# Performance work log

Hardware: AMD Instinct MI355X
Metric: run time of the kernel (lower is better)

## Reference

```python
import jax, jax.numpy as jnp
import numpy as np

N_NODES = 100000
N_EDGES = 3200000
N_GRAPHS = 2048
MOL_DIM = 78
HID = 32
OUT = 128
N_LAYERS = 5
BN_EPS = 1e-5


def setup_inputs() -> dict:
    key = jax.random.key(0)
    ks = jax.random.split(key, 16)
    x = jax.random.normal(ks[0], (N_NODES, MOL_DIM), dtype=jnp.float32)
    edge_index = jax.random.randint(ks[1], (2, N_EDGES), 0, N_NODES, dtype=jnp.int32)
    batch = jnp.sort(jax.random.randint(ks[2], (N_NODES,), 0, N_GRAPHS, dtype=jnp.int32))
    def lin(k, fan_in, shape):
        b = 1.0 / np.sqrt(fan_in)
        return jax.random.uniform(k, shape, jnp.float32, -b, b)
    # layer 0 MLP (78 -> 32 -> 32)
    w1_0 = lin(ks[3], MOL_DIM, (MOL_DIM, HID))
    b1_0 = lin(ks[4], MOL_DIM, (HID,))
    w2_0 = lin(ks[5], HID, (HID, HID))
    b2_0 = lin(ks[6], HID, (HID,))
    # layers 1..4 MLPs (32 -> 32 -> 32), stacked
    w1 = lin(ks[7], HID, (N_LAYERS - 1, HID, HID))
    b1 = lin(ks[8], HID, (N_LAYERS - 1, HID))
    w2 = lin(ks[9], HID, (N_LAYERS - 1, HID, HID))
    b2 = lin(ks[10], HID, (N_LAYERS - 1, HID))
    # BatchNorm affine params per layer
    gamma = jnp.ones((N_LAYERS, HID), jnp.float32)
    beta = jnp.zeros((N_LAYERS, HID), jnp.float32)
    # final fc (32 -> 128)
    fc_w = lin(ks[11], HID, (HID, OUT))
    fc_b = lin(ks[12], HID, (OUT,))
    return {"x": x, "edge_index": edge_index, "batch": batch,
            "w1_0": w1_0, "b1_0": b1_0, "w2_0": w2_0, "b2_0": b2_0,
            "w1": w1, "b1": b1, "w2": w2, "b2": b2,
            "gamma": gamma, "beta": beta, "fc_w": fc_w, "fc_b": fc_b}


def _gin_layer(x, src, dst, W1, B1, W2, B2, g, bt):
    # GIN aggregation: (1+eps)*x + sum_{j in N(i)} x_j, eps = 0
    agg = x + jax.ops.segment_sum(x[src], dst, num_segments=N_NODES)
    h = jnp.maximum(agg @ W1 + B1, 0.0)   # Linear + ReLU
    h = h @ W2 + B2                        # Linear
    h = jnp.maximum(h, 0.0)                # outer act before BN
    mean = jnp.mean(h, axis=0)
    var = jnp.mean(jnp.square(h - mean), axis=0)  # biased (training BN)
    return (h - mean) * jax.lax.rsqrt(var + BN_EPS) * g + bt


def reference(x, edge_index, batch, w1_0, b1_0, w2_0, b2_0,
              w1, b1, w2, b2, gamma, beta, fc_w, fc_b):
    src, dst = edge_index[0], edge_index[1]
    h = _gin_layer(x, src, dst, w1_0, b1_0, w2_0, b2_0, gamma[0], beta[0])
    for i in range(N_LAYERS - 1):
        h = _gin_layer(h, src, dst, w1[i], b1[i], w2[i], b2[i],
                       gamma[i + 1], beta[i + 1])
    pooled = jax.ops.segment_sum(h, batch, num_segments=N_GRAPHS)  # [G, HID]
    out = jnp.maximum(pooled @ fc_w + fc_b, 0.0)  # dropout is identity in eval
    return out
```

## Files before the change

kernel.cpp:

```cpp
#include <hip/hip_runtime.h>
#include <hip/hip_fp16.h>

#define N_NODES 100000
#define N_EDGES 3200000
#define N_GRAPHS 2048
#define MOL 78
#define HID 32
#define OUTD 128
#define BN_EPS 1e-5f

#define NBUCK ((N_NODES + 255) / 256)
#define BCAP2 9216
#define EPB 4096
#define P1_BLOCKS ((N_EDGES + EPB - 1) / EPB)

#define NPH 4
#define CPL_BLOCKS (N_NODES / (8 * NPH))

#define NCOPY 64

__device__ inline unsigned int pkh2(float a, float b) {
    __half2 h = __halves2half2(__float2half_rn(a), __float2half_rn(b));
    return *(unsigned int*)&h;
}
__device__ inline float hlo(unsigned int v) {
    __half2 h = *(__half2*)&v;
    return __low2float(h);
}
__device__ inline float hhi(unsigned int v) {
    __half2 h = *(__half2*)&v;
    return __high2float(h);
}


__global__ __launch_bounds__(256) void part1_kernel(const int* __restrict__ src,
                                                    const int* __restrict__ dst,
                                                    int* __restrict__ gcur,
                                                    int* __restrict__ staging) {
    __shared__ int hist[NBUCK];
    __shared__ int lofs[NBUCK];
    __shared__ int lcur[NBUCK];
    __shared__ int gb[NBUCK];
    __shared__ int pk[EPB];
    __shared__ unsigned short bkt[EPB];
    __shared__ int sc[256];
    const int t = threadIdx.x;
    const int base = blockIdx.x * EPB;
    const int nedge = min(EPB, N_EDGES - base);

    for (int i = t; i < NBUCK; i += 256) hist[i] = 0;
    __syncthreads();
    for (int i = t; i < nedge; i += 256) atomicAdd(&hist[dst[base + i] >> 8], 1);
    __syncthreads();

    int a0 = (2 * t < NBUCK) ? hist[2 * t] : 0;
    int a1 = (2 * t + 1 < NBUCK) ? hist[2 * t + 1] : 0;
    int tot = a0 + a1;
    sc[t] = tot;
    __syncthreads();
    for (int off = 1; off < 256; off <<= 1) {
        int add = (t >= off) ? sc[t - off] : 0;
        __syncthreads();
        sc[t] += add;
        __syncthreads();
    }
    int excl = sc[t] - tot;
    if (2 * t < NBUCK) { lofs[2 * t] = excl; lcur[2 * t] = excl; }
    if (2 * t + 1 < NBUCK) { lofs[2 * t + 1] = excl + a0; lcur[2 * t + 1] = excl + a0; }
    __syncthreads();

    for (int i = t; i < nedge; i += 256) {
        int d = dst[base + i];
        int s = src[base + i];
        int b = d >> 8;
        int p = atomicAdd(&lcur[b], 1);
        pk[p] = (s << 8) | (d & 255);
        bkt[p] = (unsigned short)b;
    }
    __syncthreads();

    for (int b = t; b < NBUCK; b += 256) {
        int c = lcur[b] - lofs[b];
        gb[b] = c ? atomicAdd(&gcur[b], c) : 0;
    }
    __syncthreads();

    for (int i = t; i < nedge; i += 256) {
        int b = bkt[i];
        staging[(size_t)b * BCAP2 + gb[b] + (i - lofs[b])] = pk[i];
    }
}

__global__ void csrbase_kernel(const int* __restrict__ gcur, int* __restrict__ bbase,
                               int* __restrict__ row_start) {
    int t = threadIdx.x;
    int a0 = (2 * t < NBUCK) ? gcur[2 * t] : 0;
    int a1 = (2 * t + 1 < NBUCK) ? gcur[2 * t + 1] : 0;
    int tot = a0 + a1;
    __shared__ int sc[256];
    sc[t] = tot;
    __syncthreads();
    for (int off = 1; off < 256; off <<= 1) {
        int add = (t >= off) ? sc[t - off] : 0;
        __syncthreads();
        sc[t] += add;
        __syncthreads();
    }
    int excl = sc[t] - tot;
    if (2 * t < NBUCK) bbase[2 * t] = excl;
    if (2 * t + 1 < NBUCK) bbase[2 * t + 1] = excl + a0;
    if (t == 0) row_start[N_NODES] = N_EDGES;
}

__global__ __launch_bounds__(256) void part2_kernel(const int* __restrict__ gcur,
                                                    const int* __restrict__ bbase,
                                                    const int* __restrict__ staging,
                                                    int* __restrict__ row_start,
                                                    int* __restrict__ csr,
                                                    float* __restrict__ degf) {
    int b = blockIdx.x, t = threadIdx.x;
    __shared__ int ldeg[256];
    __shared__ int lex[256];
    __shared__ int sc[256];
    ldeg[t] = 0;
    __syncthreads();
    int cnt = gcur[b];
    int base = bbase[b];
    const int* sp = staging + (size_t)b * BCAP2;
    for (int i = t; i < cnt; i += 256) atomicAdd(&ldeg[sp[i] & 255], 1);
    __syncthreads();
    int v = ldeg[t];
    sc[t] = v;
    __syncthreads();
    for (int off = 1; off < 256; off <<= 1) {
        int add = (t >= off) ? sc[t - off] : 0;
        __syncthreads();
        sc[t] += add;
        __syncthreads();
    }
    int excl = sc[t] - v;
    int node = b * 256 + t;
    if (node < N_NODES) {
        row_start[node] = base + excl;
        degf[node] = 1.0f + (float)v;
    }
    lex[t] = base + excl;
    __syncthreads();
    for (int i = t; i < cnt; i += 256) {
        int pk = sp[i];
        int p = atomicAdd(&lex[pk & 255], 1);
        csr[p] = pk >> 8;
    }
}


__global__ void gcnt_kernel(const int* __restrict__ batch, int* __restrict__ cnt) {
    int g = blockIdx.x * blockDim.x + threadIdx.x;
    if (g >= N_GRAPHS) return;
    auto lb = [&](int key) {
        int lo = 0, hi = N_NODES;
        while (lo < hi) {
            int mid = (lo + hi) >> 1;
            if (batch[mid] < key) lo = mid + 1; else hi = mid;
        }
        return lo;
    };
    cnt[g] = lb(g + 1) - lb(g);
}


__global__ __launch_bounds__(256) void proj78_kernel(const float* __restrict__ in,
                                                     const float* __restrict__ W1,
                                                     unsigned int* __restrict__ y) {
    __shared__ float w1s[MOL * HID];
    for (int i = threadIdx.x; i < MOL * HID; i += 256) w1s[i] = W1[i];
    __syncthreads();
    const int node = blockIdx.x * 256 + threadIdx.x;
    if (node >= N_NODES) return;
    const float* row = in + (size_t)node * MOL;
    float acc[HID];
#pragma unroll
    for (int j = 0; j < HID; j++) acc[j] = 0.f;
    const float4* w1v = (const float4*)w1s;
    for (int k = 0; k < MOL; k++) {
        float xv = row[k];
#pragma unroll
        for (int q = 0; q < 8; q++) {
            float4 wv = w1v[k * 8 + q];
            acc[4 * q + 0] = fmaf(xv, wv.x, acc[4 * q + 0]);
            acc[4 * q + 1] = fmaf(xv, wv.y, acc[4 * q + 1]);
            acc[4 * q + 2] = fmaf(xv, wv.z, acc[4 * q + 2]);
            acc[4 * q + 3] = fmaf(xv, wv.w, acc[4 * q + 3]);
        }
    }
    uint4* o = (uint4*)(y + (size_t)node * 16);
#pragma unroll
    for (int g = 0; g < 4; g++) {
        uint4 u;
        u.x = pkh2(acc[8 * g + 0], acc[8 * g + 1]);
        u.y = pkh2(acc[8 * g + 2], acc[8 * g + 3]);
        u.z = pkh2(acc[8 * g + 4], acc[8 * g + 5]);
        u.w = pkh2(acc[8 * g + 6], acc[8 * g + 7]);
        o[g] = u;
    }
}


__global__ __launch_bounds__(256) void agg_kernel(const unsigned int* __restrict__ y,
                                                  const int* __restrict__ rs,
                                                  const int* __restrict__ csr,
                                                  float* __restrict__ agg) {
    int gt = blockIdx.x * blockDim.x + threadIdx.x;
    int node = gt >> 5;
    if (node >= N_NODES) return;
    int hl = threadIdx.x & 31;
    int s = hl >> 2;
    int q = hl & 3;
    const uint4* rows = (const uint4*)y;
    float acc[8];
#pragma unroll
    for (int i = 0; i < 8; i++) acc[i] = 0.f;
    if (s == 0) {
        uint4 u = rows[(size_t)node * 4 + q];
        acc[0] = hlo(u.x); acc[1] = hhi(u.x);
        acc[2] = hlo(u.y); acc[3] = hhi(u.y);
        acc[4] = hlo(u.z); acc[5] = hhi(u.z);
        acc[6] = hlo(u.w); acc[7] = hhi(u.w);
    }
    int e0 = rs[node], e1 = rs[node + 1];
    int k = e0 + s;
    for (; k + 8 < e1; k += 16) {
        uint4 a = rows[(size_t)csr[k] * 4 + q];
        uint4 b = rows[(size_t)csr[k + 8] * 4 + q];
        acc[0] += hlo(a.x) + hlo(b.x);
        acc[1] += hhi(a.x) + hhi(b.x);
        acc[2] += hlo(a.y) + hlo(b.y);
        acc[3] += hhi(a.y) + hhi(b.y);
        acc[4] += hlo(a.z) + hlo(b.z);
        acc[5] += hhi(a.z) + hhi(b.z);
        acc[6] += hlo(a.w) + hlo(b.w);
        acc[7] += hhi(a.w) + hhi(b.w);
    }
    if (k < e1) {
        uint4 a = rows[(size_t)csr[k] * 4 + q];
        acc[0] += hlo(a.x); acc[1] += hhi(a.x);
        acc[2] += hlo(a.y); acc[3] += hhi(a.y);
        acc[4] += hlo(a.z); acc[5] += hhi(a.z);
        acc[6] += hlo(a.w); acc[7] += hhi(a.w);
    }
#pragma unroll
    for (int m = 4; m <= 16; m <<= 1) {
#pragma unroll
        for (int i = 0; i < 8; i++) acc[i] += __shfl_xor(acc[i], m, 32);
    }
    if (s == 0) {
        float4* o = (float4*)(agg + (size_t)node * HID + q * 8);
        o[0] = make_float4(acc[0], acc[1], acc[2], acc[3]);
        o[1] = make_float4(acc[4], acc[5], acc[6], acc[7]);
    }
}


__global__ __launch_bounds__(256) void mlp2cpl_kernel(const float* __restrict__ agg,
                                                      const float* __restrict__ B1,
                                                      const float* __restrict__ W2,
                                                      const float* __restrict__ B2,
                                                      __half* __restrict__ out,
                                                      float* __restrict__ sums) {
    __shared__ float ldsv[8][NPH][HID];
    __shared__ float ssum[64];
    const int t = threadIdx.x;
    const int hw = t >> 5;
    const int c = t & 31;
    if (t < 64) ssum[t] = 0.f;
    float w2col[32];
#pragma unroll
    for (int k = 0; k < 32; k++) w2col[k] = W2[k * 32 + c];
    const float b1c = B1[c], b2c = B2[c];
    const int n0 = (blockIdx.x * 8 + hw) * NPH;
#pragma unroll
    for (int u = 0; u < NPH; u++) {
        float v = fmaxf(agg[(size_t)(n0 + u) * 32 + c] + b1c, 0.f);
        ldsv[hw][u][c] = v;
    }
    __syncthreads();
    float sl = 0.f, sq = 0.f;
#pragma unroll
    for (int u = 0; u < NPH; u++) {
        float h = b2c;
        const float4* vv4 = (const float4*)&ldsv[hw][u][0];
#pragma unroll
        for (int q = 0; q < 8; q++) {
            float4 vv = vv4[q];
            h = fmaf(vv.x, w2col[4 * q + 0], h);
            h = fmaf(vv.y, w2col[4 * q + 1], h);
            h = fmaf(vv.z, w2col[4 * q + 2], h);
            h = fmaf(vv.w, w2col[4 * q + 3], h);
        }
        h = fmaxf(h, 0.f);
        out[(size_t)(n0 + u) * 32 + c] = __float2half_rn(h);
        sl += h;
        sq += h * h;
    }
    atomicAdd(&ssum[c], sl);
    atomicAdd(&ssum[32 + c], sq);
    __syncthreads();
    if (t < 64) atomicAdd(&sums[(blockIdx.x & (NCOPY - 1)) * 64 + t], ssum[t]);
}


template <bool LAST>
__global__ __launch_bounds__(256) void fusedmlp_kernel(
    const float* __restrict__ aggh, const float* __restrict__ degf,
    const float* __restrict__ scsh_prev, const float* __restrict__ B1,
    const float* __restrict__ W1, const float* __restrict__ W2, const float* __restrict__ B2,
    __half* __restrict__ out, float* __restrict__ sums, const int* __restrict__ batch,
    float* __restrict__ pooledraw) {
    __shared__ float ldsu[8][NPH][HID];
    __shared__ float ldsv[8][HID];
    __shared__ float ssum[64];
    const int t = threadIdx.x;
    const int hw = t >> 5;
    const int c = t & 31;
    if (t < 64) ssum[t] = 0.f;
    float w1col[32], w2col[32];
#pragma unroll
    for (int k = 0; k < 32; k++) {
        w1col[k] = W1[k * 32 + c];
        w2col[k] = W2[k * 32 + c];
    }
    const float scv = scsh_prev[c], shv = scsh_prev[HID + c];
    const float b1c = B1[c], b2c = B2[c];
    const int n0 = (blockIdx.x * 8 + hw) * NPH;
#pragma unroll
    for (int u = 0; u < NPH; u++) {
        int n = n0 + u;
        float cdeg = degf[n];
        ldsu[hw][u][c] = fmaf(aggh[(size_t)n * 32 + c], scv, cdeg * shv);
    }
    __syncthreads();
    float sl = 0.f, sq = 0.f;
#pragma unroll
    for (int u = 0; u < NPH; u++) {
        const int n = n0 + u;
        float tv = b1c;
        const float4* uu4 = (const float4*)&ldsu[hw][u][0];
#pragma unroll
        for (int q = 0; q < 8; q++) {
            float4 uu = uu4[q];
            tv = fmaf(uu.x, w1col[4 * q + 0], tv);
            tv = fmaf(uu.y, w1col[4 * q + 1], tv);
            tv = fmaf(uu.z, w1col[4 * q + 2], tv);
            tv = fmaf(uu.w, w1col[4 * q + 3], tv);
        }
        tv = fmaxf(tv, 0.f);
        ldsv[hw][c] = tv;
        float h = b2c;
        const float4* vv4 = (const float4*)&ldsv[hw][0];
#pragma unroll
        for (int q = 0; q < 8; q++) {
            float4 vv = vv4[q];
            h = fmaf(vv.x, w2col[4 * q + 0], h);
            h = fmaf(vv.y, w2col[4 * q + 1], h);
            h = fmaf(vv.z, w2col[4 * q + 2], h);
            h = fmaf(vv.w, w2col[4 * q + 3], h);
        }
        h = fmaxf(h, 0.f);
        if (LAST) {
            atomicAdd(&pooledraw[batch[n] * HID + c], h);
        } else {
            out[(size_t)n * 32 + c] = __float2half_rn(h);
        }
        sl += h;
        sq += h * h;
    }
    atomicAdd(&ssum[c], sl);
    atomicAdd(&ssum[32 + c], sq);
    __syncthreads();
    if (t < 64) atomicAdd(&sums[(blockIdx.x & (NCOPY - 1)) * 64 + t], ssum[t]);
}


__global__ void bnfin_kernel(const float* __restrict__ sums, const float* __restrict__ g,
                             const float* __restrict__ bt, float* __restrict__ scsh) {
    __shared__ float red[64];
    int t = threadIdx.x;
    if (t < 64) {
        float acc = 0.f;
#pragma unroll 8
        for (int k = 0; k < NCOPY; k++) acc += sums[k * 64 + t];
        red[t] = acc;
    }
    __syncthreads();
    if (t < HID) {
        float m = red[t] * (1.0f / N_NODES);
        float var = red[HID + t] * (1.0f / N_NODES) - m * m;
        var = fmaxf(var, 0.f);
        float sc = g[t] * rsqrtf(var + BN_EPS);
        scsh[t] = sc;
        scsh[HID + t] = bt[t] - m * sc;
    }
}


__global__ void fc_kernel(const float* __restrict__ praw, const int* __restrict__ cnt,
                          const float* __restrict__ scsh4, const float* __restrict__ fcw,
                          const float* __restrict__ fcb, float* __restrict__ out) {
    __shared__ float w[HID * OUTD];
    __shared__ float aff[2 * HID];
    for (int i = threadIdx.x; i < HID * OUTD; i += 256) w[i] = fcw[i];
    if (threadIdx.x < 2 * HID) aff[threadIdx.x] = scsh4[threadIdx.x];
    __syncthreads();
    int idx = blockIdx.x * 256 + threadIdx.x;
    if (idx >= N_GRAPHS * OUTD) return;
    int g = idx >> 7;
    int o = idx & 127;
    float cg = (float)cnt[g];
    float acc = fcb[o];
#pragma unroll
    for (int k = 0; k < HID; k++) {
        float paff = fmaf(praw[g * HID + k], aff[k], cg * aff[HID + k]);
        acc = fmaf(paff, w[k * OUTD + o], acc);
    }
    out[idx] = fmaxf(acc, 0.f);
}


extern "C" void kernel_launch(void* const* d_in, const int* in_sizes, int n_in,
                              void* d_out, int out_size, void* d_ws, size_t ws_size,
                              hipStream_t stream) {
    const float* x = (const float*)d_in[0];
    const int* ei = (const int*)d_in[1];
    const int* batch = (const int*)d_in[2];
    const float* w1_0 = (const float*)d_in[3];
    const float* b1_0 = (const float*)d_in[4];
    const float* w2_0 = (const float*)d_in[5];
    const float* b2_0 = (const float*)d_in[6];
    const float* w1 = (const float*)d_in[7];
    const float* b1 = (const float*)d_in[8];
    const float* w2 = (const float*)d_in[9];
    const float* b2 = (const float*)d_in[10];
    const float* gamma = (const float*)d_in[11];
    const float* beta = (const float*)d_in[12];
    const float* fc_w = (const float*)d_in[13];
    const float* fc_b = (const float*)d_in[14];
    float* out = (float*)d_out;

    const int* e_src = ei;
    const int* e_dst = ei + N_EDGES;

    char* ws = (char*)d_ws;
    size_t off = 0;
    auto alloc = [&](size_t n) {
        void* p = ws + off;
        off += (n + 255) & ~(size_t)255;
        return p;
    };
    int* row_start = (int*)alloc((size_t)(N_NODES + 1) * 4);
    int* csr = (int*)alloc((size_t)N_EDGES * 4);
    int* bbase = (int*)alloc((size_t)NBUCK * 4);
    int* staging = (int*)alloc((size_t)NBUCK * BCAP2 * 4);
    unsigned int* ybuf = (unsigned int*)alloc((size_t)N_NODES * 16 * 4);
    float* aggb = (float*)alloc((size_t)N_NODES * HID * 4);
    __half* hbuf = (__half*)alloc((size_t)N_NODES * HID * 2);
    float* degf = (float*)alloc((size_t)N_NODES * 4);
    float* scsh = (float*)alloc(5 * 2 * HID * 4);
    int* cnt = (int*)alloc((size_t)N_GRAPHS * 4);
    size_t zero_base = off;
    int* gcur = (int*)alloc((size_t)NBUCK * 4);
    float* bnsums = (float*)alloc((size_t)5 * NCOPY * 64 * 4);
    float* pooled = (float*)alloc((size_t)N_GRAPHS * HID * 4);
    size_t zero_len = off - zero_base;

    hipMemsetAsync(ws + zero_base, 0, zero_len, stream);

    part1_kernel<<<P1_BLOCKS, 256, 0, stream>>>(e_src, e_dst, gcur, staging);
    csrbase_kernel<<<1, 256, 0, stream>>>(gcur, bbase, row_start);
    part2_kernel<<<NBUCK, 256, 0, stream>>>(gcur, bbase, staging, row_start, csr, degf);
    gcnt_kernel<<<(N_GRAPHS + 255) / 256, 256, 0, stream>>>(batch, cnt);

    const int nodeBlocks = (N_NODES + 255) / 256;
    const int aggBlocks = (N_NODES * 32 + 255) / 256;

    proj78_kernel<<<nodeBlocks, 256, 0, stream>>>(x, w1_0, ybuf);
    agg_kernel<<<aggBlocks, 256, 0, stream>>>(ybuf, row_start, csr, aggb);
    mlp2cpl_kernel<<<CPL_BLOCKS, 256, 0, stream>>>(aggb, b1_0, w2_0, b2_0, hbuf, bnsums);
    bnfin_kernel<<<1, 64, 0, stream>>>(bnsums, gamma, beta, scsh);

    for (int l = 1; l < 5; l++) {
        int i = l - 1;
        agg_kernel<<<aggBlocks, 256, 0, stream>>>((const unsigned int*)hbuf, row_start, csr,
                                                  aggb);
        if (l < 4) {
            fusedmlp_kernel<false><<<CPL_BLOCKS, 256, 0, stream>>>(
                aggb, degf, scsh + (l - 1) * 2 * HID, b1 + (size_t)i * HID,
                w1 + (size_t)i * HID * HID, w2 + (size_t)i * HID * HID, b2 + (size_t)i * HID,
                hbuf, bnsums + (size_t)l * NCOPY * 64, nullptr, nullptr);
        } else {
            fusedmlp_kernel<true><<<CPL_BLOCKS, 256, 0, stream>>>(
                aggb, degf, scsh + (l - 1) * 2 * HID, b1 + (size_t)i * HID,
                w1 + (size_t)i * HID * HID, w2 + (size_t)i * HID * HID, b2 + (size_t)i * HID,
                nullptr, bnsums + (size_t)l * NCOPY * 64, batch, pooled);
        }
        bnfin_kernel<<<1, 64, 0, stream>>>(bnsums + (size_t)l * NCOPY * 64, gamma + l * HID,
                                           beta + l * HID, scsh + l * 2 * HID);
    }

    fc_kernel<<<(N_GRAPHS * OUTD + 255) / 256, 256, 0, stream>>>(
        pooled, cnt, scsh + 4 * 2 * HID, fc_w, fc_b, out);
}
```

Baseline: 424.4 us.

## Fuse neighbor aggregation into per-layer MLP kernel with ping-pong fp16 buffers

Merges the separate gather-sum aggregation kernel into the MLP/BatchNorm-statistics kernel. Each half-wave now gathers its 4 nodes' neighbors and writes the BN-adjusted or bias+ReLU row straight into shared memory. This removes the fp32 aggregation buffer round trip through global memory and one launch per layer, and alternates two fp16 feature buffers between layers. In exchange, each half-wave processes its nodes' gathers one after another, which may reduce memory-level parallelism. The removed block barrier before the shared-sum atomics also introduces a possible race on their initialisation.

```diff
diff --git a/kernel.cpp b/kernel.cpp
--- a/kernel.cpp
+++ b/kernel.cpp
@@ -206,167 +206,150 @@
 }
 
 
-__global__ __launch_bounds__(256) void agg_kernel(const unsigned int* __restrict__ y,
-                                                  const int* __restrict__ rs,
-                                                  const int* __restrict__ csr,
-                                                  float* __restrict__ agg) {
-    int gt = blockIdx.x * blockDim.x + threadIdx.x;
-    int node = gt >> 5;
-    if (node >= N_NODES) return;
-    int hl = threadIdx.x & 31;
-    int s = hl >> 2;
-    int q = hl & 3;
-    const uint4* rows = (const uint4*)y;
-    float acc[8];
-#pragma unroll
-    for (int i = 0; i < 8; i++) acc[i] = 0.f;
-    if (s == 0) {
-        uint4 u = rows[(size_t)node * 4 + q];
-        acc[0] = hlo(u.x); acc[1] = hhi(u.x);
-        acc[2] = hlo(u.y); acc[3] = hhi(u.y);
-        acc[4] = hlo(u.z); acc[5] = hhi(u.z);
-        acc[6] = hlo(u.w); acc[7] = hhi(u.w);
-    }
-    int e0 = rs[node], e1 = rs[node + 1];
-    int k = e0 + s;
-    for (; k + 8 < e1; k += 16) {
-        uint4 a = rows[(size_t)csr[k] * 4 + q];
-        uint4 b = rows[(size_t)csr[k + 8] * 4 + q];
-        acc[0] += hlo(a.x) + hlo(b.x);
-        acc[1] += hhi(a.x) + hhi(b.x);
-        acc[2] += hlo(a.y) + hlo(b.y);
-        acc[3] += hhi(a.y) + hhi(b.y);
-        acc[4] += hlo(a.z) + hlo(b.z);
-        acc[5] += hhi(a.z) + hhi(b.z);
-        acc[6] += hlo(a.w) + hlo(b.w);
-        acc[7] += hhi(a.w) + hhi(b.w);
-    }
-    if (k < e1) {
-        uint4 a = rows[(size_t)csr[k] * 4 + q];
-        acc[0] += hlo(a.x); acc[1] += hhi(a.x);
-        acc[2] += hlo(a.y); acc[3] += hhi(a.y);
-        acc[4] += hlo(a.z); acc[5] += hhi(a.z);
-        acc[6] += hlo(a.w); acc[7] += hhi(a.w);
-    }
-#pragma unroll
-    for (int m = 4; m <= 16; m <<= 1) {
-#pragma unroll
-        for (int i = 0; i < 8; i++) acc[i] += __shfl_xor(acc[i], m, 32);
-    }
-    if (s == 0) {
-        float4* o = (float4*)(agg + (size_t)node * HID + q * 8);
-        o[0] = make_float4(acc[0], acc[1], acc[2], acc[3]);
-        o[1] = make_float4(acc[4], acc[5], acc[6], acc[7]);
-    }
-}
-
-
-__global__ __launch_bounds__(256) void mlp2cpl_kernel(const float* __restrict__ agg,
-                                                      const float* __restrict__ B1,
-                                                      const float* __restrict__ W2,
-                                                      const float* __restrict__ B2,
-                                                      __half* __restrict__ out,
-                                                      float* __restrict__ sums) {
-    __shared__ float ldsv[8][NPH][HID];
-    __shared__ float ssum[64];
-    const int t = threadIdx.x;
-    const int hw = t >> 5;
-    const int c = t & 31;
-    if (t < 64) ssum[t] = 0.f;
-    float w2col[32];
-#pragma unroll
-    for (int k = 0; k < 32; k++) w2col[k] = W2[k * 32 + c];
-    const float b1c = B1[c], b2c = B2[c];
-    const int n0 = (blockIdx.x * 8 + hw) * NPH;
-#pragma unroll
-    for (int u = 0; u < NPH; u++) {
-        float v = fmaxf(agg[(size_t)(n0 + u) * 32 + c] + b1c, 0.f);
-        ldsv[hw][u][c] = v;
-    }
-    __syncthreads();
-    float sl = 0.f, sq = 0.f;
-#pragma unroll
-    for (int u = 0; u < NPH; u++) {
-        float h = b2c;
-        const float4* vv4 = (const float4*)&ldsv[hw][u][0];
-#pragma unroll
-        for (int q = 0; q < 8; q++) {
-            float4 vv = vv4[q];
-            h = fmaf(vv.x, w2col[4 * q + 0], h);
-            h = fmaf(vv.y, w2col[4 * q + 1], h);
-            h = fmaf(vv.z, w2col[4 * q + 2], h);
-            h = fmaf(vv.w, w2col[4 * q + 3], h);
-        }
-        h = fmaxf(h, 0.f);
-        out[(size_t)(n0 + u) * 32 + c] = __float2half_rn(h);
-        sl += h;
-        sq += h * h;
-    }
-    atomicAdd(&ssum[c], sl);
-    atomicAdd(&ssum[32 + c], sq);
-    __syncthreads();
-    if (t < 64) atomicAdd(&sums[(blockIdx.x & (NCOPY - 1)) * 64 + t], ssum[t]);
-}
-
-
-template <bool LAST>
-__global__ __launch_bounds__(256) void fusedmlp_kernel(
-    const float* __restrict__ aggh, const float* __restrict__ degf,
-    const float* __restrict__ scsh_prev, const float* __restrict__ B1,
-    const float* __restrict__ W1, const float* __restrict__ W2, const float* __restrict__ B2,
-    __half* __restrict__ out, float* __restrict__ sums, const int* __restrict__ batch,
-    float* __restrict__ pooledraw) {
+template <int MODE>
+__global__ __launch_bounds__(256) void gma_kernel(
+    const unsigned int* __restrict__ y, const int* __restrict__ rs, const int* __restrict__ csr,
+    const float* __restrict__ degf, const float* __restrict__ scsh_prev,
+    const float* __restrict__ B1, const float* __restrict__ W1, const float* __restrict__ W2,
+    const float* __restrict__ B2, __half* __restrict__ out, float* __restrict__ sums,
+    const int* __restrict__ batch, float* __restrict__ pooledraw) {
     __shared__ float ldsu[8][NPH][HID];
     __shared__ float ldsv[8][HID];
     __shared__ float ssum[64];
     const int t = threadIdx.x;
     const int hw = t >> 5;
-    const int c = t & 31;
+    const int hl = t & 31;
+    const int s = hl >> 2;
+    const int q = hl & 3;
+    const int c = hl;
     if (t < 64) ssum[t] = 0.f;
-    float w1col[32], w2col[32];
-#pragma unroll
-    for (int k = 0; k < 32; k++) {
-        w1col[k] = W1[k * 32 + c];
-        w2col[k] = W2[k * 32 + c];
-    }
-    const float scv = scsh_prev[c], shv = scsh_prev[HID + c];
-    const float b1c = B1[c], b2c = B2[c];
+
+    float4 p0a, p0b, p1a, p1b;
+    if (MODE == 0) {
+        p0a = ((const float4*)B1)[2 * q];
+        p0b = ((const float4*)B1)[2 * q + 1];
+    } else {
+        p0a = ((const float4*)scsh_prev)[2 * q];
+        p0b = ((const float4*)scsh_prev)[2 * q + 1];
+        p1a = ((const float4*)(scsh_prev + HID))[2 * q];
+        p1b = ((const float4*)(scsh_prev + HID))[2 * q + 1];
+    }
+
     const int n0 = (blockIdx.x * 8 + hw) * NPH;
-#pragma unroll
-    for (int u = 0; u < NPH; u++) {
-        int n = n0 + u;
-        float cdeg = degf[n];
-        ldsu[hw][u][c] = fmaf(aggh[(size_t)n * 32 + c], scv, cdeg * shv);
-    }
-    __syncthreads();
-    float sl = 0.f, sq = 0.f;
-#pragma unroll
+    const uint4* rows = (const uint4*)y;
+
     for (int u = 0; u < NPH; u++) {
         const int n = n0 + u;
-        float tv = b1c;
+        float acc[8];
+#pragma unroll
+        for (int i = 0; i < 8; i++) acc[i] = 0.f;
+        if (s == 0) {
+            uint4 w = rows[(size_t)n * 4 + q];
+            acc[0] = hlo(w.x); acc[1] = hhi(w.x);
+            acc[2] = hlo(w.y); acc[3] = hhi(w.y);
+            acc[4] = hlo(w.z); acc[5] = hhi(w.z);
+            acc[6] = hlo(w.w); acc[7] = hhi(w.w);
+        }
+        int e0 = rs[n], e1 = rs[n + 1];
+        int k = e0 + s;
+        for (; k + 8 < e1; k += 16) {
+            uint4 a = rows[(size_t)csr[k] * 4 + q];
+            uint4 b = rows[(size_t)csr[k + 8] * 4 + q];
+            acc[0] += hlo(a.x) + hlo(b.x);
+            acc[1] += hhi(a.x) + hhi(b.x);
+            acc[2] += hlo(a.y) + hlo(b.y);
+            acc[3] += hhi(a.y) + hhi(b.y);
+            acc[4] += hlo(a.z) + hlo(b.z);
+            acc[5] += hhi(a.z) + hhi(b.z);
+            acc[6] += hlo(a.w) + hlo(b.w);
+            acc[7] += hhi(a.w) + hhi(b.w);
+        }
+        if (k < e1) {
+            uint4 a = rows[(size_t)csr[k] * 4 + q];
+            acc[0] += hlo(a.x); acc[1] += hhi(a.x);
+            acc[2] += hlo(a.y); acc[3] += hhi(a.y);
+            acc[4] += hlo(a.z); acc[5] += hhi(a.z);
+            acc[6] += hlo(a.w); acc[7] += hhi(a.w);
+        }
+#pragma unroll
+        for (int m = 4; m <= 16; m <<= 1) {
+#pragma unroll
+            for (int i = 0; i < 8; i++) acc[i] += __shfl_xor(acc[i], m, 32);
+        }
+        if (s == 0) {
+            float o[8];
+            if (MODE == 0) {
+                o[0] = fmaxf(acc[0] + p0a.x, 0.f); o[1] = fmaxf(acc[1] + p0a.y, 0.f);
+                o[2] = fmaxf(acc[2] + p0a.z, 0.f); o[3] = fmaxf(acc[3] + p0a.w, 0.f);
+                o[4] = fmaxf(acc[4] + p0b.x, 0.f); o[5] = fmaxf(acc[5] + p0b.y, 0.f);
+                o[6] = fmaxf(acc[6] + p0b.z, 0.f); o[7] = fmaxf(acc[7] + p0b.w, 0.f);
+            } else {
+                float dn = degf[n];
+                o[0] = fmaf(acc[0], p0a.x, dn * p1a.x);
+                o[1] = fmaf(acc[1], p0a.y, dn * p1a.y);
+                o[2] = fmaf(acc[2], p0a.z, dn * p1a.z);
+                o[3] = fmaf(acc[3], p0a.w, dn * p1a.w);
+                o[4] = fmaf(acc[4], p0b.x, dn * p1b.x);
+                o[5] = fmaf(acc[5], p0b.y, dn * p1b.y);
+                o[6] = fmaf(acc[6], p0b.z, dn * p1b.z);
+                o[7] = fmaf(acc[7], p0b.w, dn * p1b.w);
+            }
+            float4* d = (float4*)&ldsu[hw][u][q * 8];
+            d[0] = make_float4(o[0], o[1], o[2], o[3]);
+            d[1] = make_float4(o[4], o[5], o[6], o[7]);
+        }
+    }
+
+    float w2col[32];
+#pragma unroll
+    for (int k = 0; k < 32; k++) w2col[k] = W2[k * 32 + c];
+    float w1col[32];
+    if (MODE != 0) {
+#pragma unroll
+        for (int k = 0; k < 32; k++) w1col[k] = W1[k * 32 + c];
+    }
+    const float b1c = (MODE != 0) ? B1[c] : 0.f;
+    const float b2c = B2[c];
+    float sl = 0.f, sq = 0.f;
+    for (int u = 0; u < NPH; u++) {
+        const int n = n0 + u;
         const float4* uu4 = (const float4*)&ldsu[hw][u][0];
-#pragma unroll
-        for (int q = 0; q < 8; q++) {
-            float4 uu = uu4[q];
-            tv = fmaf(uu.x, w1col[4 * q + 0], tv);
-            tv = fmaf(uu.y, w1col[4 * q + 1], tv);
-            tv = fmaf(uu.z, w1col[4 * q + 2], tv);
-            tv = fmaf(uu.w, w1col[4 * q + 3], tv);
-        }
-        tv = fmaxf(tv, 0.f);
-        ldsv[hw][c] = tv;
-        float h = b2c;
-        const float4* vv4 = (const float4*)&ldsv[hw][0];
-#pragma unroll
-        for (int q = 0; q < 8; q++) {
-            float4 vv = vv4[q];
-            h = fmaf(vv.x, w2col[4 * q + 0], h);
-            h = fmaf(vv.y, w2col[4 * q + 1], h);
-            h = fmaf(vv.z, w2col[4 * q + 2], h);
-            h = fmaf(vv.w, w2col[4 * q + 3], h);
+        float h;
+        if (MODE == 0) {
+            h = b2c;
+#pragma unroll
+            for (int qq = 0; qq < 8; qq++) {
+                float4 vv = uu4[qq];
+                h = fmaf(vv.x, w2col[4 * qq + 0], h);
+                h = fmaf(vv.y, w2col[4 * qq + 1], h);
+                h = fmaf(vv.z, w2col[4 * qq + 2], h);
+                h = fmaf(vv.w, w2col[4 * qq + 3], h);
+            }
+        } else {
+            float tv = b1c;
+#pragma unroll
+            for (int qq = 0; qq < 8; qq++) {
+                float4 uu = uu4[qq];
+                tv = fmaf(uu.x, w1col[4 * qq + 0], tv);
+                tv = fmaf(uu.y, w1col[4 * qq + 1], tv);
+                tv = fmaf(uu.z, w1col[4 * qq + 2], tv);
+                tv = fmaf(uu.w, w1col[4 * qq + 3], tv);
+            }
+            tv = fmaxf(tv, 0.f);
+            ldsv[hw][c] = tv;
+            h = b2c;
+            const float4* vv4 = (const float4*)&ldsv[hw][0];
+#pragma unroll
+            for (int qq = 0; qq < 8; qq++) {
+                float4 vv = vv4[qq];
+                h = fmaf(vv.x, w2col[4 * qq + 0], h);
+                h = fmaf(vv.y, w2col[4 * qq + 1], h);
+                h = fmaf(vv.z, w2col[4 * qq + 2], h);
+                h = fmaf(vv.w, w2col[4 * qq + 3], h);
+            }
         }
         h = fmaxf(h, 0.f);
-        if (LAST) {
+        if (MODE == 2) {
             atomicAdd(&pooledraw[batch[n] * HID + c], h);
         } else {
             out[(size_t)n * 32 + c] = __float2half_rn(h);
@@ -460,9 +443,8 @@
     int* csr = (int*)alloc((size_t)N_EDGES * 4);
     int* bbase = (int*)alloc((size_t)NBUCK * 4);
     int* staging = (int*)alloc((size_t)NBUCK * BCAP2 * 4);
-    unsigned int* ybuf = (unsigned int*)alloc((size_t)N_NODES * 16 * 4);
-    float* aggb = (float*)alloc((size_t)N_NODES * HID * 4);
-    __half* hbuf = (__half*)alloc((size_t)N_NODES * HID * 2);
+    unsigned int* hA = (unsigned int*)alloc((size_t)N_NODES * 16 * 4);
+    unsigned int* hB = (unsigned int*)alloc((size_t)N_NODES * 16 * 4);
     float* degf = (float*)alloc((size_t)N_NODES * 4);
     float* scsh = (float*)alloc(5 * 2 * HID * 4);
     int* cnt = (int*)alloc((size_t)N_GRAPHS * 4);
@@ -480,25 +462,26 @@
     gcnt_kernel<<<(N_GRAPHS + 255) / 256, 256, 0, stream>>>(batch, cnt);
 
     const int nodeBlocks = (N_NODES + 255) / 256;
-    const int aggBlocks = (N_NODES * 32 + 255) / 256;
-
-    proj78_kernel<<<nodeBlocks, 256, 0, stream>>>(x, w1_0, ybuf);
-    agg_kernel<<<aggBlocks, 256, 0, stream>>>(ybuf, row_start, csr, aggb);
-    mlp2cpl_kernel<<<CPL_BLOCKS, 256, 0, stream>>>(aggb, b1_0, w2_0, b2_0, hbuf, bnsums);
+
+    proj78_kernel<<<nodeBlocks, 256, 0, stream>>>(x, w1_0, hA);
+    gma_kernel<0><<<CPL_BLOCKS, 256, 0, stream>>>(
+        hA, row_start, csr, nullptr, nullptr, b1_0, nullptr, w2_0, b2_0, (__half*)hB, bnsums,
+        nullptr, nullptr);
     bnfin_kernel<<<1, 64, 0, stream>>>(bnsums, gamma, beta, scsh);
 
+    unsigned int* cur = hB;
+    unsigned int* nxt = hA;
     for (int l = 1; l < 5; l++) {
         int i = l - 1;
-        agg_kernel<<<aggBlocks, 256, 0, stream>>>((const unsigned int*)hbuf, row_start, csr,
-                                                  aggb);
         if (l < 4) {
-            fusedmlp_kernel<false><<<CPL_BLOCKS, 256, 0, stream>>>(
-                aggb, degf, scsh + (l - 1) * 2 * HID, b1 + (size_t)i * HID,
+            gma_kernel<1><<<CPL_BLOCKS, 256, 0, stream>>>(
+                cur, row_start, csr, degf, scsh + (l - 1) * 2 * HID, b1 + (size_t)i * HID,
                 w1 + (size_t)i * HID * HID, w2 + (size_t)i * HID * HID, b2 + (size_t)i * HID,
-                hbuf, bnsums + (size_t)l * NCOPY * 64, nullptr, nullptr);
+                (__half*)nxt, bnsums + (size_t)l * NCOPY * 64, nullptr, nullptr);
+            unsigned int* tmp = cur; cur = nxt; nxt = tmp;
         } else {
-            fusedmlp_kernel<true><<<CPL_BLOCKS, 256, 0, stream>>>(
-                aggb, degf, scsh + (l - 1) * 2 * HID, b1 + (size_t)i * HID,
+            gma_kernel<2><<<CPL_BLOCKS, 256, 0, stream>>>(
+                cur, row_start, csr, degf, scsh + (l - 1) * 2 * HID, b1 + (size_t)i * HID,
                 w1 + (size_t)i * HID * HID, w2 + (size_t)i * HID * HID, b2 + (size_t)i * HID,
                 nullptr, bnsums + (size_t)l * NCOPY * 64, batch, pooled);
         }
```

Result: no change. 421.3 us (-0.7%).
